# Kernel optimization log

Hardware: AMD Instinct MI355X
Metric: run time of the kernel (lower is better)

The kernel has to match this reference:

```python
import jax, jax.numpy as jnp
import numpy as np

B, T = 4096, 512
H1, H2 = 512, 512
NUM_CLASSES = 20
FORGET_BIAS = 1.0  # TF LSTMCell default


def _lstm_step(c, h, x, W, b):
    # TF LSTMCell: concat([x, h]) @ W + b, split into i, j, f, o
    z = jnp.concatenate([x, h], axis=-1) @ W + b
    i, j, f, o = jnp.split(z, 4, axis=-1)
    new_c = c * jax.nn.sigmoid(f + FORGET_BIAS) + jax.nn.sigmoid(i) * jnp.tanh(j)
    new_h = jnp.tanh(new_c) * jax.nn.sigmoid(o)
    return new_c, new_h


def setup_inputs() -> dict:
    key = jax.random.key(0)
    ks = jax.random.split(key, 7)
    s1 = 1.0 / np.sqrt(1 + H1)
    s2 = 1.0 / np.sqrt(H1 + H2)
    s3 = 1.0 / np.sqrt(H2)
    return {
        "x": jax.random.normal(ks[0], (B, T), dtype=jnp.float32),
        "W1": jax.random.normal(ks[1], (1 + H1, 4 * H1), dtype=jnp.float32) * s1,
        "b1": jnp.zeros((4 * H1,), dtype=jnp.float32),
        "W2": jax.random.normal(ks[2], (H1 + H2, 4 * H2), dtype=jnp.float32) * s2,
        "b2": jnp.zeros((4 * H2,), dtype=jnp.float32),
        "softmax_w": jax.random.normal(ks[3], (H2, NUM_CLASSES), dtype=jnp.float32) * s3,
        "softmax_b": jnp.full((NUM_CLASSES,), 0.1, dtype=jnp.float32),
    }


def reference(x, W1, b1, W2, b2, softmax_w, softmax_b):
    xs = x.T[:, :, None]  # [T, B, 1] — each timestep is a scalar feature

    def step(carry, x_t):
        c1, h1, c2, h2 = carry
        c1, h1 = _lstm_step(c1, h1, x_t, W1, b1)
        c2, h2 = _lstm_step(c2, h2, h1, W2, b2)
        return (c1, h1, c2, h2), None

    z = jnp.zeros((x.shape[0],), dtype=x.dtype)
    init = (jnp.zeros((x.shape[0], H1), x.dtype), jnp.zeros((x.shape[0], H1), x.dtype),
            jnp.zeros((x.shape[0], H2), x.dtype), jnp.zeros((x.shape[0], H2), x.dtype))
    (c1, h1, c2, h2), _ = jax.lax.scan(step, init, xs)

    logits = h2 @ softmax_w + softmax_b
    class_probabilities = jax.nn.softmax(logits, axis=-1)
    predicted_classes = jnp.argmax(logits, axis=1).astype(jnp.int32)
    return logits, class_probabilities, predicted_classes
```

## Files before the change

### kernel.cpp

```cpp
#include <hip/hip_runtime.h>
#include <math.h>

#define BATCH 4096
#define TSTEPS 512
#define HID 512
#define NCLS 20

typedef __attribute__((ext_vector_type(8))) short short8;
typedef __attribute__((ext_vector_type(4))) float float4v;
typedef unsigned short ushort_t;
typedef unsigned int uint32;

__device__ __forceinline__ float sigmoidf_(float x){ return 1.0f/(1.0f+expf(-x)); }

__device__ __forceinline__ ushort_t f2bf(float f){
  union { float f; uint32 u; } v; v.f = f;
  return (ushort_t)((v.u + 0x7fffu + ((v.u>>16)&1u)) >> 16);
}
__device__ __forceinline__ float bf2f(ushort_t h){
  union { float f; uint32 u; } v; v.u = ((uint32)h)<<16; return v.f;
}

__device__ __forceinline__ void gload16(const void* g, void* l){
  __builtin_amdgcn_global_load_lds(
      (const __attribute__((address_space(1))) uint32*)g,
      (__attribute__((address_space(3))) uint32*)l, 16, 0, 0);
}

template<int K>
__global__ __launch_bounds__(256) void prep_w_k(const float* __restrict__ W, int row0,
                                                ushort_t* __restrict__ Whi, ushort_t* __restrict__ Wlo)
{
  __shared__ float s[32][33];
  const int cx = blockIdx.x;
  const int cy = blockIdx.y;
  const int tid = threadIdx.x;
  #pragma unroll
  for (int i = 0; i < 4; ++i) {
    int idx = tid + i*256;
    int kk = idx >> 5, nn = idx & 31;
    s[kk][nn] = W[(size_t)(row0 + cy*32 + kk)*2048 + cx*32 + nn];
  }
  __syncthreads();
  #pragma unroll
  for (int i = 0; i < 4; ++i) {
    int idx = tid + i*256;
    int nn = idx >> 5, kk = idx & 31;
    float v = s[kk][nn];
    ushort_t hi = f2bf(v);
    ushort_t lo = f2bf(v - bf2f(hi));
    size_t o = (size_t)(cx*32+nn)*K + cy*32 + kk;
    Whi[o] = hi; Wlo[o] = lo;
  }
}

template<int KTOT, bool HASX>
__global__ __launch_bounds__(256) void lstm_step_mfma(
    const ushort_t* __restrict__ A0hi, const ushort_t* __restrict__ A0lo,
    const ushort_t* __restrict__ A1hi, const ushort_t* __restrict__ A1lo,
    const ushort_t* __restrict__ Bhi,  const ushort_t* __restrict__ Blo,
    const float* __restrict__ bias, const float* __restrict__ wxrow,
    const float* __restrict__ x, int t,
    float* __restrict__ c,
    ushort_t* __restrict__ Hhi, ushort_t* __restrict__ Hlo)
{
  __shared__ ushort_t sAhi[128*64];
  __shared__ ushort_t sAlo[128*64];
  __shared__ ushort_t sBhi[128*64];
  __shared__ ushort_t sBlo[128*64];
  __shared__ float sX[128];

  const int tid  = threadIdx.x;
  const int lane = tid & 63;
  const int wave = tid >> 6;
  const int wm   = wave >> 1;
  const int wu   = wave & 1;
  const int u0   = blockIdx.x * 32;
  const int b0   = blockIdx.y * 128;

  if (HASX) { if (tid < 128) sX[tid] = x[(size_t)(b0 + tid)*TSTEPS + t]; }

  float4v acc[4][4];
  #pragma unroll
  for (int mi = 0; mi < 4; ++mi)
    #pragma unroll
    for (int g = 0; g < 4; ++g) acc[mi][g] = (float4v)0.f;

  const int srow = lane >> 3;
  const int sch  = ((lane & 7) ^ (lane >> 3)) * 8;

  for (int kt = 0; kt < KTOT; kt += 64) {
    const ushort_t* Ah; const ushort_t* Al; int kk;
    if (KTOT > 512 && kt >= 512) { Ah = A1hi; Al = A1lo; kk = kt - 512; }
    else                         { Ah = A0hi; Al = A0lo; kk = kt; }

    #pragma unroll
    for (int i = 0; i < 4; ++i) {
      const int j  = i*8 + srow;
      const int br = b0 + wave*32 + j;
      const int wr = wave*512 + u0 + j;
      gload16(Ah  + (size_t)br*HID  + kk + sch, &sAhi[(wave*32 + i*8)*64]);
      gload16(Al  + (size_t)br*HID  + kk + sch, &sAlo[(wave*32 + i*8)*64]);
      gload16(Bhi + (size_t)wr*KTOT + kt + sch, &sBhi[(wave*32 + i*8)*64]);
      gload16(Blo + (size_t)wr*KTOT + kt + sch, &sBlo[(wave*32 + i*8)*64]);
    }
    __syncthreads();

    #pragma unroll
    for (int ks = 0; ks < 2; ++ks) {
      const int chR = ((ks*4 + (lane >> 4)) ^ (lane & 7)) * 8;
      short8 a_hi[4], a_lo[4], b_hi[4], b_lo[4];
      #pragma unroll
      for (int mi = 0; mi < 4; ++mi) {
        int off = (wm*64 + mi*16 + (lane & 15))*64 + chR;
        a_hi[mi] = *(const short8*)&sAhi[off];
        a_lo[mi] = *(const short8*)&sAlo[off];
      }
      #pragma unroll
      for (int g = 0; g < 4; ++g) {
        int off = (g*32 + wu*16 + (lane & 15))*64 + chR;
        b_hi[g] = *(const short8*)&sBhi[off];
        b_lo[g] = *(const short8*)&sBlo[off];
      }
      #pragma unroll
      for (int mi = 0; mi < 4; ++mi)
        #pragma unroll
        for (int g = 0; g < 4; ++g) {
          acc[mi][g] = __builtin_amdgcn_mfma_f32_16x16x32_bf16(a_hi[mi], b_hi[g], acc[mi][g], 0,0,0);
          acc[mi][g] = __builtin_amdgcn_mfma_f32_16x16x32_bf16(a_hi[mi], b_lo[g], acc[mi][g], 0,0,0);
          acc[mi][g] = __builtin_amdgcn_mfma_f32_16x16x32_bf16(a_lo[mi], b_hi[g], acc[mi][g], 0,0,0);
        }
    }
    __syncthreads();
  }

  const int ul = u0 + wu*16 + (lane & 15);
  float bb[4], wx[4];
  #pragma unroll
  for (int g = 0; g < 4; ++g) bb[g] = bias[g*512 + ul];
  if (HASX) {
    #pragma unroll
    for (int g = 0; g < 4; ++g) wx[g] = wxrow[g*512 + ul];
  }
  #pragma unroll
  for (int mi = 0; mi < 4; ++mi) {
    #pragma unroll
    for (int r = 0; r < 4; ++r) {
      int b = b0 + wm*64 + mi*16 + (lane >> 4)*4 + r;
      float zi = acc[mi][0][r] + bb[0];
      float zj = acc[mi][1][r] + bb[1];
      float zf = acc[mi][2][r] + bb[2];
      float zo = acc[mi][3][r] + bb[3];
      if (HASX) {
        float xv = sX[b - b0];
        zi += xv*wx[0]; zj += xv*wx[1]; zf += xv*wx[2]; zo += xv*wx[3];
      }
      size_t off = (size_t)b*HID + ul;
      float cv = c[off];
      float cn = cv * sigmoidf_(zf + 1.0f) + sigmoidf_(zi)*tanhf(zj);
      c[off] = cn;
      float hn = tanhf(cn)*sigmoidf_(zo);
      ushort_t hi = f2bf(hn);
      ushort_t lo = f2bf(hn - bf2f(hi));
      Hhi[off] = hi; Hlo[off] = lo;
    }
  }
}

__global__ __launch_bounds__(256) void head_k(
    const ushort_t* __restrict__ h2hi, const ushort_t* __restrict__ h2lo,
    const float* __restrict__ sw, const float* __restrict__ sb, float* __restrict__ out)
{
  int wid  = (blockIdx.x * blockDim.x + threadIdx.x) >> 6;
  int lane = threadIdx.x & 63;
  if (wid >= BATCH) return;
  float acc[NCLS];
  #pragma unroll
  for (int cc = 0; cc < NCLS; ++cc) acc[cc] = 0.f;
  for (int u = lane; u < HID; u += 64) {
    size_t off = (size_t)wid*HID + u;
    float hv = bf2f(h2hi[off]) + bf2f(h2lo[off]);
    #pragma unroll
    for (int cc = 0; cc < NCLS; ++cc) acc[cc] += hv * sw[(size_t)u*NCLS + cc];
  }
  #pragma unroll
  for (int cc = 0; cc < NCLS; ++cc) {
    #pragma unroll
    for (int off = 32; off > 0; off >>= 1) acc[cc] += __shfl_down(acc[cc], off);
  }
  if (lane == 0) {
    float logits[NCLS];
    float mx = -1e30f;
    #pragma unroll
    for (int cc = 0; cc < NCLS; ++cc) { logits[cc] = acc[cc] + sb[cc]; mx = fmaxf(mx, logits[cc]); }
    float ex[NCLS]; float s = 0.f;
    #pragma unroll
    for (int cc = 0; cc < NCLS; ++cc) { ex[cc] = expf(logits[cc] - mx); s += ex[cc]; }
    float inv = 1.f / s;
    int best = 0; float bv = logits[0];
    #pragma unroll
    for (int cc = 1; cc < NCLS; ++cc) { if (logits[cc] > bv) { bv = logits[cc]; best = cc; } }
    float* lo = out;
    float* pr = out + (size_t)BATCH*NCLS;
    float* pc = out + (size_t)2*BATCH*NCLS;
    #pragma unroll
    for (int cc = 0; cc < NCLS; ++cc) {
      lo[(size_t)wid*NCLS + cc] = logits[cc];
      pr[(size_t)wid*NCLS + cc] = ex[cc]*inv;
    }
    pc[wid] = (float)best;
  }
}

extern "C" void kernel_launch(void* const* d_in, const int* in_sizes, int n_in,
                              void* d_out, int out_size, void* d_ws, size_t ws_size,
                              hipStream_t stream) {
  const float* x  = (const float*)d_in[0];
  const float* W1 = (const float*)d_in[1];
  const float* b1 = (const float*)d_in[2];
  const float* W2 = (const float*)d_in[3];
  const float* b2 = (const float*)d_in[4];
  const float* sw = (const float*)d_in[5];
  const float* sb = (const float*)d_in[6];
  float* out = (float*)d_out;

  ushort_t* p = (ushort_t*)d_ws;
  const size_t S = (size_t)BATCH * HID;
  ushort_t* W1thi = p;                  p += 2048*512;
  ushort_t* W1tlo = p;                  p += 2048*512;
  ushort_t* W2thi = p;                  p += 2048*1024;
  ushort_t* W2tlo = p;                  p += 2048*1024;
  ushort_t* h1hi[2] = { p, p + S };     p += 2*S;
  ushort_t* h1lo[2] = { p, p + S };     p += 2*S;
  ushort_t* h2hi[2] = { p, p + S };     p += 2*S;
  ushort_t* h2lo[2] = { p, p + S };     p += 2*S;
  float* c1 = (float*)p;
  float* c2 = c1 + S;

  prep_w_k<512> <<<dim3(64,16), 256, 0, stream>>>(W1, 1, W1thi, W1tlo);
  prep_w_k<1024><<<dim3(64,32), 256, 0, stream>>>(W2, 0, W2thi, W2tlo);

  hipMemsetAsync(h1hi[0], 0, S*sizeof(ushort_t), stream);
  hipMemsetAsync(h1lo[0], 0, S*sizeof(ushort_t), stream);
  hipMemsetAsync(h2hi[0], 0, S*sizeof(ushort_t), stream);
  hipMemsetAsync(h2lo[0], 0, S*sizeof(ushort_t), stream);
  hipMemsetAsync(c1,      0, S*sizeof(float),    stream);
  hipMemsetAsync(c2,      0, S*sizeof(float),    stream);

  dim3 grid(HID/32, BATCH/128);
  for (int t = 0; t < TSTEPS; ++t) {
    int cur = t & 1, nxt = cur ^ 1;
    lstm_step_mfma<512,  true ><<<grid, 256, 0, stream>>>(
        h1hi[cur], h1lo[cur], nullptr, nullptr,
        W1thi, W1tlo, b1, W1 , x, t,
        c1, h1hi[nxt], h1lo[nxt]);
    lstm_step_mfma<1024, false><<<grid, 256, 0, stream>>>(
        h1hi[nxt], h1lo[nxt], h2hi[cur], h2lo[cur],
        W2thi, W2tlo, b2, nullptr, nullptr, 0,
        c2, h2hi[nxt], h2lo[nxt]);
  }
  head_k<<<1024, 256, 0, stream>>>(h2hi[0], h2lo[0], sw, sb, out);
}
```

Measured before the change: 41.07 ms.

## Double-buffer LDS tiles to overlap global loads with MFMA compute

```diff
diff --git a/kernel.cpp b/kernel.cpp
--- a/kernel.cpp
+++ b/kernel.cpp
@@ -64,10 +64,10 @@
     float* __restrict__ c,
     ushort_t* __restrict__ Hhi, ushort_t* __restrict__ Hlo)
 {
-  __shared__ ushort_t sAhi[128*64];
-  __shared__ ushort_t sAlo[128*64];
-  __shared__ ushort_t sBhi[128*64];
-  __shared__ ushort_t sBlo[128*64];
+  __shared__ ushort_t sAhi[2][128*64];
+  __shared__ ushort_t sAlo[2][128*64];
+  __shared__ ushort_t sBhi[2][128*64];
+  __shared__ ushort_t sBlo[2][128*64];
   __shared__ float sX[128];
 
   const int tid  = threadIdx.x;
@@ -89,22 +89,36 @@
   const int srow = lane >> 3;
   const int sch  = ((lane & 7) ^ (lane >> 3)) * 8;
 
-  for (int kt = 0; kt < KTOT; kt += 64) {
+  auto stage = [&](int bs, int kt){
     const ushort_t* Ah; const ushort_t* Al; int kk;
     if (KTOT > 512 && kt >= 512) { Ah = A1hi; Al = A1lo; kk = kt - 512; }
     else                         { Ah = A0hi; Al = A0lo; kk = kt; }
-
     #pragma unroll
     for (int i = 0; i < 4; ++i) {
       const int j  = i*8 + srow;
       const int br = b0 + wave*32 + j;
       const int wr = wave*512 + u0 + j;
-      gload16(Ah  + (size_t)br*HID  + kk + sch, &sAhi[(wave*32 + i*8)*64]);
-      gload16(Al  + (size_t)br*HID  + kk + sch, &sAlo[(wave*32 + i*8)*64]);
-      gload16(Bhi + (size_t)wr*KTOT + kt + sch, &sBhi[(wave*32 + i*8)*64]);
-      gload16(Blo + (size_t)wr*KTOT + kt + sch, &sBlo[(wave*32 + i*8)*64]);
-    }
-    __syncthreads();
+      const int ld = (wave*32 + i*8)*64;
+      gload16(Ah  + (size_t)br*HID  + kk + sch, &sAhi[bs][ld]);
+      gload16(Al  + (size_t)br*HID  + kk + sch, &sAlo[bs][ld]);
+      gload16(Bhi + (size_t)wr*KTOT + kt + sch, &sBhi[bs][ld]);
+      gload16(Blo + (size_t)wr*KTOT + kt + sch, &sBlo[bs][ld]);
+    }
+  };
+
+  constexpr int NK = KTOT / 64;
+  stage(0, 0);
+
+  for (int kt64 = 0; kt64 < NK; ++kt64) {
+    const int cur = kt64 & 1;
+    if (kt64 + 1 < NK) {
+      stage(cur ^ 1, (kt64 + 1) * 64);
+      asm volatile("s_waitcnt vmcnt(16)" ::: "memory");
+    } else {
+      asm volatile("s_waitcnt vmcnt(0)" ::: "memory");
+    }
+    __builtin_amdgcn_s_barrier();
+    __builtin_amdgcn_sched_barrier(0);
 
     #pragma unroll
     for (int ks = 0; ks < 2; ++ks) {
@@ -113,14 +127,14 @@
       #pragma unroll
       for (int mi = 0; mi < 4; ++mi) {
         int off = (wm*64 + mi*16 + (lane & 15))*64 + chR;
-        a_hi[mi] = *(const short8*)&sAhi[off];
-        a_lo[mi] = *(const short8*)&sAlo[off];
+        a_hi[mi] = *(const short8*)&sAhi[cur][off];
+        a_lo[mi] = *(const short8*)&sAlo[cur][off];
       }
       #pragma unroll
       for (int g = 0; g < 4; ++g) {
         int off = (g*32 + wu*16 + (lane & 15))*64 + chR;
-        b_hi[g] = *(const short8*)&sBhi[off];
-        b_lo[g] = *(const short8*)&sBlo[off];
+        b_hi[g] = *(const short8*)&sBhi[cur][off];
+        b_lo[g] = *(const short8*)&sBlo[cur][off];
       }
       #pragma unroll
       for (int mi = 0; mi < 4; ++mi)
@@ -131,7 +145,8 @@
           acc[mi][g] = __builtin_amdgcn_mfma_f32_16x16x32_bf16(a_lo[mi], b_hi[g], acc[mi][g], 0,0,0);
         }
     }
-    __syncthreads();
+    __builtin_amdgcn_sched_barrier(0);
+    __builtin_amdgcn_s_barrier();
   }
 
   const int ul = u0 + wu*16 + (lane & 15);
```

New measurement: 63.20 ms. +53.9%, slower.
